# Kernel tuning notes

Hardware: AMD Instinct MI355X
Metric: run time of the kernel (lower is better)

## Reference

```python
import jax, jax.numpy as jnp
import numpy as np

B, N, INC, H, W = 1, 6, 256, 56, 100
DD, CC = 41, 64                         # depth bins (4..45 step 1), cam feat channels
NX, NY, NZ = 33, 33, 2                  # BEV grid from pc_range=[-50,-50,-5,50,50,3], grid=3
CZ = CC * NZ                            # 128 channels into bevencode
DXV = jnp.array([3.0, 3.0, 3.0], jnp.float32)
BXV = jnp.array([-48.5, -48.5, -3.5], jnp.float32)


def _frustum():
    ds = jnp.arange(4.0, 45.0, 1.0)                      # (41,)
    xs = jnp.linspace(0.0, 1599.0, W)
    ys = jnp.linspace(0.0, 899.0, H)
    d = jnp.broadcast_to(ds[:, None, None], (DD, H, W))
    xg = jnp.broadcast_to(xs[None, None, :], (DD, H, W))
    yg = jnp.broadcast_to(ys[None, :, None], (DD, H, W))
    return jnp.stack([xg, yg, d], -1)                    # (D,H,W,3)


def _conv(x, w):
    return jax.lax.conv_general_dilated(x, w, (1, 1), 'SAME',
                                        dimension_numbers=('NCHW', 'OIHW', 'NCHW'))


def _bn_relu(x, s, b, m, v):
    inv = s / jnp.sqrt(v + 1e-5)
    return jax.nn.relu(x * inv[None, :, None, None] + (b - m * inv)[None, :, None, None])


def _forward(x, rots, trans, dn_w, dn_b,
             bw1, bn1_s, bn1_b, bn1_m, bn1_v,
             bw2, bn2_s, bn2_b, bn2_m, bn2_v,
             bw3, bn3_s, bn3_b, bn3_m, bn3_v,
             bw4, bn4_s, bn4_b, bn4_m, bn4_v):
    # ---- CamEncode: 1x1 depthnet -> softmax depth dist + context features ----
    xf = x.reshape(B * N, INC, H, W)
    y = _conv(xf, dn_w) + dn_b[None, :, None, None]
    depth = jax.nn.softmax(y[:, :DD], axis=1).reshape(B, N, DD, H, W)
    feat = y[:, DD:DD + CC].reshape(B, N, CC, H, W)
    # ---- get_geometry: (u*d, v*d, d) -> ego frame ----
    fr = _frustum()                                                     # (D,H,W,3)
    pts = jnp.concatenate([fr[..., :2] * fr[..., 2:3], fr[..., 2:3]], -1)
    geom = jnp.einsum('bnij,dhwj->bndhwi', rots, pts) + trans[:, :, None, None, None, :]
    # ---- voxel indices (torch .long() truncates toward zero) ----
    coor = ((geom - (BXV - DXV / 2.0)) / DXV).astype(jnp.int32)         # (B,N,D,H,W,3)
    cx, cy, cz = coor[..., 0], coor[..., 1], coor[..., 2]
    kept = (cx >= 0) & (cx < NX) & (cy >= 0) & (cy < NY) & (cz >= 0) & (cz < NZ)
    bidx = jnp.arange(B, dtype=jnp.int32)[:, None, None, None, None]
    ranks = ((bidx * NZ + cz) * NY + cy) * NX + cx                      # bev rank per point
    nvox = B * NZ * NY * NX
    seg = jnp.where(kept, ranks, nvox).reshape(-1)                      # drop bucket = nvox
    # ---- lift: depth-weighted outer product, splat: segment-sum by voxel ----
    vol = depth[..., None] * feat.transpose(0, 1, 3, 4, 2)[:, :, None]  # (B,N,D,H,W,C)
    bev = jax.ops.segment_sum(vol.reshape(-1, CC), seg, num_segments=nvox + 1)[:nvox]
    bev = bev.reshape(B, NZ, NY, NX, CC).transpose(0, 4, 1, 2, 3).reshape(B, CZ, NY, NX)
    h = _bn_relu(_conv(bev, bw1), bn1_s, bn1_b, bn1_m, bn1_v)
    h = _bn_relu(_conv(h, bw2), bn2_s, bn2_b, bn2_m, bn2_v)
    h = _bn_relu(_conv(h, bw3), bn3_s, bn3_b, bn3_m, bn3_v)
    h = _bn_relu(_conv(h, bw4), bn4_s, bn4_b, bn4_m, bn4_v)
    return h                                                            # (B,256,33,33)


def setup_inputs() -> dict:
    key = jax.random.key(0)
    ks = jax.random.split(key, 16)
    x = jax.random.normal(ks[0], (B, N, INC, H, W), jnp.float32)
    # rots = small rotation perturbation composed with intrinsics inverse
    kinv = jnp.array([[1.0 / 800.0, 0.0, -1.0], [0.0, 1.0 / 800.0, -0.5625], [0.0, 0.0, 1.0]], jnp.float32)
    R = jnp.eye(3, dtype=jnp.float32) + 0.05 * jax.random.normal(ks[1], (B, N, 3, 3), jnp.float32)
    rots = jnp.einsum('bnij,jk->bnik', R, kinv)
    trans = 2.0 * jax.random.normal(ks[2], (B, N, 3), jnp.float32)

    def w(k, o, i, kh, kw):
        return jax.random.normal(k, (o, i, kh, kw), jnp.float32) * (2.0 / (i * kh * kw)) ** 0.5

    def bn(k, c):
        k1, k2, k3, k4 = jax.random.split(k, 4)
        return (1.0 + 0.1 * jax.random.normal(k1, (c,), jnp.float32),
                0.1 * jax.random.normal(k2, (c,), jnp.float32),
                0.1 * jax.random.normal(k3, (c,), jnp.float32),
                jax.random.uniform(k4, (c,), jnp.float32, 0.5, 1.5))
    bn1 = bn(ks[7], CZ); bn2 = bn(ks[8], 512); bn3 = bn(ks[9], 512); bn4 = bn(ks[10], 256)
    return dict(
        x=x, rots=rots, trans=trans,
        dn_w=w(ks[3], DD + CC, INC, 1, 1), dn_b=jnp.zeros((DD + CC,), jnp.float32),
        bw1=w(ks[4], CZ, CZ, 3, 3),
        bn1_s=bn1[0], bn1_b=bn1[1], bn1_m=bn1[2], bn1_v=bn1[3],
        bw2=w(ks[5], 512, CZ, 3, 3),
        bn2_s=bn2[0], bn2_b=bn2[1], bn2_m=bn2[2], bn2_v=bn2[3],
        bw3=w(ks[6], 512, 512, 3, 3),
        bn3_s=bn3[0], bn3_b=bn3[1], bn3_m=bn3[2], bn3_v=bn3[3],
        bw4=w(ks[11], 256, 512, 3, 3),
        bn4_s=bn4[0], bn4_b=bn4[1], bn4_m=bn4[2], bn4_v=bn4[3])


def reference(x, rots, trans, dn_w, dn_b,
              bw1, bn1_s, bn1_b, bn1_m, bn1_v,
              bw2, bn2_s, bn2_b, bn2_m, bn2_v,
              bw3, bn3_s, bn3_b, bn3_m, bn3_v,
              bw4, bn4_s, bn4_b, bn4_m, bn4_v):
    return _forward(x, rots, trans, dn_w, dn_b,
                    bw1, bn1_s, bn1_b, bn1_m, bn1_v,
                    bw2, bn2_s, bn2_b, bn2_m, bn2_v,
                    bw3, bn3_s, bn3_b, bn3_m, bn3_v,
                    bw4, bn4_s, bn4_b, bn4_m, bn4_v)
```

## Files before the change

kernel.cpp:

```cpp
#include <hip/hip_runtime.h>
#include <math.h>

#define NCAM  6
#define INC   256
#define HH    56
#define WW    100
#define HW    5600
#define NPIX  33600
#define DDEP  41
#define CFEAT 64
#define NCH   105
#define NXG   33
#define NYG   33
#define NZG   2
#define NVOX  2178
#define PADW  35
#define PADHW 1225
#define NPIXO 1089

typedef short bf16x8 __attribute__((ext_vector_type(8)));
typedef float f32x4  __attribute__((ext_vector_type(4)));

#define Y_OFF    0
#define YW_SZ    3538944
#define W3H_OFF  (Y_OFF)
#define W3L_OFF  (W3H_OFF + 1179648)
#define W4H_OFF  (W3L_OFF + 1179648)
#define W4L_OFF  (W4H_OFF + 589824)
#define W12_OFF  (Y_OFF + YW_SZ)
#define W1H_OFF  (W12_OFF)
#define W1L_OFF  (W1H_OFF + 73728)
#define W2H_OFF  (W1L_OFF + 73728)
#define W2L_OFF  (W2H_OFF + 294912)
#define BEV_OFF  (W2L_OFF + 294912)
#define BEV_SZ   (NVOX * CFEAT)
#define A0H_OFF  (BEV_OFF + BEV_SZ)
#define A0L_OFF  (A0H_OFF + 78400)
#define A1H_OFF  (A0L_OFF + 78400)
#define A1L_OFF  (A1H_OFF + 78400)
#define A2H_OFF  (A1L_OFF + 78400)
#define A2L_OFF  (A2H_OFF + 313600)
#define A3H_OFF  (A2L_OFF + 313600)
#define A3L_OFF  (A3H_OFF + 313600)
#define P_OFF    (A3L_OFF + 313600)
#define P_SZ     4460544
#define WS_END   (P_OFF + P_SZ)
#define WDH_OFF  (P_OFF)
#define WDL_OFF  (P_OFF + 16384)

__device__ __forceinline__ unsigned short f2bf_rn(float f) {
    unsigned u = __builtin_bit_cast(unsigned, f);
    unsigned r = (u + 0x7FFFu + ((u >> 16) & 1u)) >> 16;
    return (unsigned short)r;
}
__device__ __forceinline__ void split_bf(float f, unsigned short& h, unsigned short& l) {
    h = f2bf_rn(f);
    float hf = __builtin_bit_cast(float, (unsigned)h << 16);
    l = f2bf_rn(f - hf);
}

__global__ __launch_bounds__(256) void k_wprep_dn(const float* __restrict__ dnw,
                                                  unsigned short* __restrict__ wdh,
                                                  unsigned short* __restrict__ wdl)
{
    int i = blockIdx.x * 256 + threadIdx.x;
    if (i >= 128 * 256) return;
    int jj = i & 7, lane = (i >> 3) & 63, chk = (i >> 9) & 7, ct = i >> 12;
    int co = ct * 16 + (lane & 15);
    int ci = chk * 32 + (lane >> 4) * 8 + jj;
    float w = (co < NCH) ? dnw[co * 256 + ci] : 0.f;
    unsigned short h, l; split_bf(w, h, l);
    wdh[i] = h; wdl[i] = l;
}

__global__ __launch_bounds__(256) void k_depthnet_direct(const float* __restrict__ x,
                                                         const unsigned short* __restrict__ wdh,
                                                         const unsigned short* __restrict__ wdl,
                                                         const float* __restrict__ dnb,
                                                         float* __restrict__ y)
{
    const int t  = threadIdx.x;
    const int w  = t >> 6;
    const int l  = t & 63;
    const int lp = l & 15;
    const int q  = l >> 4;
    const int n   = blockIdx.y;
    const int ct0 = blockIdx.z * 4;
    const int px  = blockIdx.x * 64 + w * 16 + lp;
    const bool pok = px < HW;
    const float* xl = x + (size_t)n * INC * HW + (pok ? px : 0);

    f32x4 acc[4];
#pragma unroll
    for (int ct = 0; ct < 4; ++ct) acc[ct] = (f32x4){0.f, 0.f, 0.f, 0.f};

#pragma unroll 2
    for (int ci0 = 0; ci0 < INC; ci0 += 32) {
        float bv[8];
#pragma unroll
        for (int jj = 0; jj < 8; ++jj)
            bv[jj] = xl[(size_t)(ci0 + q * 8 + jj) * HW];
        bf16x8 Bh, Bl;
#pragma unroll
        for (int jj = 0; jj < 8; ++jj) {
            unsigned short h, lo; split_bf(pok ? bv[jj] : 0.f, h, lo);
            Bh[jj] = (short)h; Bl[jj] = (short)lo;
        }
#pragma unroll
        for (int ct = 0; ct < 4; ++ct) {
            const size_t ab = (size_t)(((ct0 + ct) * 8 + (ci0 >> 5)) * 64 + l) * 8;
            bf16x8 Ah = *(const bf16x8*)&wdh[ab];
            bf16x8 Al = *(const bf16x8*)&wdl[ab];
            acc[ct] = __builtin_amdgcn_mfma_f32_16x16x32_bf16(Ah, Bh, acc[ct], 0, 0, 0);
            acc[ct] = __builtin_amdgcn_mfma_f32_16x16x32_bf16(Ah, Bl, acc[ct], 0, 0, 0);
            acc[ct] = __builtin_amdgcn_mfma_f32_16x16x32_bf16(Al, Bh, acc[ct], 0, 0, 0);
        }
    }
    if (pok) {
#pragma unroll
        for (int ct = 0; ct < 4; ++ct) {
#pragma unroll
            for (int j = 0; j < 4; ++j) {
                int co = (ct0 + ct) * 16 + q * 4 + j;
                if (co < NCH)
                    y[((size_t)n * NCH + co) * HW + px] = acc[ct][j] + dnb[co];
            }
        }
    }
}

__global__ __launch_bounds__(256) void k_softmax(float* __restrict__ y)
{
    int p = blockIdx.x * 256 + threadIdx.x;
    if (p >= NPIX) return;
    int n = p / HW, hw = p - n * HW;
    float* base = y + (size_t)n * NCH * HW + hw;
    float v[DDEP];
    float m = -3.4e38f;
#pragma unroll
    for (int d = 0; d < DDEP; ++d) { v[d] = base[(size_t)d * HW]; m = fmaxf(m, v[d]); }
    float s = 0.f;
#pragma unroll
    for (int d = 0; d < DDEP; ++d) { v[d] = expf(v[d] - m); s += v[d]; }
#pragma unroll
    for (int d = 0; d < DDEP; ++d) base[(size_t)d * HW] = v[d] / s;
}

__global__ __launch_bounds__(256) void k_splat(const float* __restrict__ y,
                                               const float* __restrict__ rots,
                                               const float* __restrict__ trans,
                                               float* __restrict__ bev)
{
    int idx = blockIdx.x * 256 + threadIdx.x;
    if (idx >= NPIX * DDEP) return;
    int di = idx / NPIX;
    int p  = idx - di * NPIX;
    int n = p / HW, hw = p - n * HW;
    int wi = hw % WW, hi = hw / WW;
    const float su = 1599.0f / 99.0f;
    const float sv = 899.0f / 55.0f;
    float u = __fmul_rn((float)wi, su);
    float v = __fmul_rn((float)hi, sv);
    const float* r = rots + n * 9;
    const float* tr = trans + n * 3;
    float dd  = 4.0f + (float)di;
    float pxv = __fmul_rn(u, dd);
    float pyv = __fmul_rn(v, dd);
    float gx = __fadd_rn(__fadd_rn(__fadd_rn(__fmul_rn(r[0], pxv), __fmul_rn(r[1], pyv)), __fmul_rn(r[2], dd)), tr[0]);
    float gy = __fadd_rn(__fadd_rn(__fadd_rn(__fmul_rn(r[3], pxv), __fmul_rn(r[4], pyv)), __fmul_rn(r[5], dd)), tr[1]);
    float gz = __fadd_rn(__fadd_rn(__fadd_rn(__fmul_rn(r[6], pxv), __fmul_rn(r[7], pyv)), __fmul_rn(r[8], dd)), tr[2]);
    int cx = (int)__fdiv_rn(__fadd_rn(gx, 50.0f), 3.0f);
    int cy = (int)__fdiv_rn(__fadd_rn(gy, 50.0f), 3.0f);
    int cz = (int)__fdiv_rn(__fadd_rn(gz, 5.0f), 3.0f);
    if (cx >= 0 && cx < NXG && cy >= 0 && cy < NYG && cz >= 0 && cz < NZG) {
        const float* dbase = y + (size_t)n * NCH * HW + hw;
        const float* fbase = dbase + (size_t)DDEP * HW;
        float dval = dbase[(size_t)di * HW];
        float* vp = bev + (size_t)((cz * NYG + cy) * NXG + cx) * CFEAT;
#pragma unroll 8
        for (int c = 0; c < CFEAT; ++c) {
            atomicAdd(vp + c, __fmul_rn(dval, fbase[(size_t)c * HW]));
        }
    }
}

__global__ __launch_bounds__(256) void k_wprep(const float* __restrict__ wgt,
                                               unsigned short* __restrict__ wh,
                                               unsigned short* __restrict__ wl,
                                               int COUT, int CIN)
{
    int i = blockIdx.x * 256 + threadIdx.x;
    int total = 9 * COUT * CIN;
    if (i >= total) return;
    int jj = i & 7, lane = (i >> 3) & 63;
    int r  = i >> 9;
    int nchk = CIN >> 5;
    int chk = r % nchk; r /= nchk;
    int ncog = COUT >> 4;
    int cog = r % ncog; int dydx = r / ncog;
    int co = cog * 16 + (lane & 15);
    int ci = chk * 32 + (lane >> 4) * 8 + jj;
    float w = wgt[((size_t)co * CIN + ci) * 9 + dydx];
    unsigned short h, l; split_bf(w, h, l);
    wh[i] = h; wl[i] = l;
}

__global__ __launch_bounds__(256) void k_bev2act(const float* __restrict__ bev,
                                                 unsigned short* __restrict__ ah,
                                                 unsigned short* __restrict__ al)
{
    int i = blockIdx.x * 256 + threadIdx.x;
    if (i >= NVOX * CFEAT) return;
    int vx = i >> 6, c = i & 63;
    int cz = vx / NPIXO, rem = vx - cz * NPIXO;
    int yy = rem / NXG, xx = rem - yy * NXG;
    int ch = c * 2 + cz;
    int pos = (yy + 1) * PADW + xx + 1;
    unsigned short h, l; split_bf(bev[i], h, l);
    ah[pos * 128 + ch] = h;
    al[pos * 128 + ch] = l;
}

template<int CIN, int COUT, int SL>
__global__ __launch_bounds__(256) void k_conv_mfma(const unsigned short* __restrict__ ah,
                                                   const unsigned short* __restrict__ al,
                                                   const unsigned short* __restrict__ wh,
                                                   const unsigned short* __restrict__ wl,
                                                   float* __restrict__ P)
{
    constexpr int CI_PER = CIN / SL;
    constexpr int NCOB = COUT / 64;
    constexpr int G    = NCOB * SL;
    constexpr int GX   = G / 8;
    constexpr int POSN = 140;
    __shared__ unsigned short bs[POSN * 64];
    const int t  = threadIdx.x;
    const int w  = t >> 6;
    const int l  = t & 63;
    const int lp = l & 15;
    const int q  = l >> 4;

    const int bid   = blockIdx.x;
    const int xcd   = bid & 7;
    const int slot  = bid >> 3;
    const int ytile = slot % 17;
    const int gon   = slot / 17;
    const int group = xcd * GX + gon;
    const int cobi  = group % NCOB;
    const int sl    = group / NCOB;

    const int y0  = ytile * 2;
    const int cob = cobi * 64 + w * 16;
    const int ci_base = sl * CI_PER;

    int  pos0[5];
    bool vld[5];
#pragma unroll
    for (int ct = 0; ct < 5; ++ct) {
        int tp = ct * 16 + lp;
        int r = tp / 33, c = tp - r * 33;
        bool v = (tp < 66) && (y0 + r < 33);
        vld[ct]  = v;
        pos0[ct] = v ? (r * 35 + c) : 0;
    }

    f32x4 acc[5];
#pragma unroll
    for (int ct = 0; ct < 5; ++ct) acc[ct] = (f32x4){0.f, 0.f, 0.f, 0.f};

    for (int chk = 0; chk < CI_PER; chk += 32) {
        const int ci0 = ci_base + chk;
        __syncthreads();
        for (int i = t; i < POSN * 8; i += 256) {
            int pos = i >> 3, s = i & 7;
            int gpos = y0 * 35 + pos;
            const unsigned short* src = (s < 4) ? ah : al;
            int sp = s ^ (pos & 7);
            uint4 val = make_uint4(0u, 0u, 0u, 0u);
            if (gpos < PADHW)
                val = *(const uint4*)&src[(size_t)gpos * CIN + ci0 + (s & 3) * 8];
            *(uint4*)&bs[pos * 64 + sp * 8] = val;
        }
        __syncthreads();

#pragma unroll 3
        for (int dydx = 0; dydx < 9; ++dydx) {
            int dy = dydx / 3, dx = dydx - dy * 3;
            int off = dy * 35 + dx;
            const size_t abase = (size_t)(((dydx * (COUT >> 4) + (cob >> 4)) * (CIN >> 5)
                                           + (ci0 >> 5)) * 64 + l) * 8;
            bf16x8 Ah = *(const bf16x8*)&wh[abase];
            bf16x8 Al = *(const bf16x8*)&wl[abase];
#pragma unroll
            for (int ct = 0; ct < 5; ++ct) {
                int pos = pos0[ct] + off;
                int sph = q ^ (pos & 7);
                bf16x8 Bh = *(const bf16x8*)&bs[pos * 64 + sph * 8];
                bf16x8 Bl = *(const bf16x8*)&bs[pos * 64 + (sph ^ 4) * 8];
                acc[ct] = __builtin_amdgcn_mfma_f32_16x16x32_bf16(Ah, Bh, acc[ct], 0, 0, 0);
                acc[ct] = __builtin_amdgcn_mfma_f32_16x16x32_bf16(Ah, Bl, acc[ct], 0, 0, 0);
                acc[ct] = __builtin_amdgcn_mfma_f32_16x16x32_bf16(Al, Bh, acc[ct], 0, 0, 0);
            }
        }
    }

#pragma unroll
    for (int ct = 0; ct < 5; ++ct) {
        if (!vld[ct]) continue;
        int gp = y0 * 33 + ct * 16 + lp;
        float* dst = P + ((size_t)sl * NPIXO + gp) * COUT + cob + q * 4;
        *(f32x4*)dst = acc[ct];
    }
}

template<int SL>
__global__ __launch_bounds__(256) void k_finish(const float* __restrict__ P,
                                                const float* __restrict__ bns,
                                                const float* __restrict__ bnb,
                                                const float* __restrict__ bnm,
                                                const float* __restrict__ bnv,
                                                unsigned short* __restrict__ oh,
                                                unsigned short* __restrict__ ol,
                                                float* __restrict__ outf,
                                                int COUT)
{
    int i = blockIdx.x * 256 + threadIdx.x;
    if (i >= COUT * NPIXO) return;
    int co = i % COUT, p = i / COUT;
    float s = 0.f;
#pragma unroll
    for (int sl = 0; sl < SL; ++sl)
        s += P[((size_t)sl * NPIXO + p) * COUT + co];
    float sc = bns[co] / sqrtf(bnv[co] + 1e-5f);
    float bi = bnb[co] - bnm[co] * sc;
    float rv = fmaxf(fmaf(s, sc, bi), 0.f);
    if (outf) {
        outf[(size_t)co * NPIXO + p] = rv;
    } else {
        int yy = p / NXG, xx = p - yy * NXG;
        int pos = (yy + 1) * PADW + xx + 1;
        unsigned short h, lo; split_bf(rv, h, lo);
        oh[(size_t)pos * COUT + co] = h;
        ol[(size_t)pos * COUT + co] = lo;
    }
}

extern "C" void kernel_launch(void* const* d_in, const int* in_sizes, int n_in,
                              void* d_out, int out_size, void* d_ws, size_t ws_size,
                              hipStream_t stream)
{
    const float* x     = (const float*)d_in[0];
    const float* rots  = (const float*)d_in[1];
    const float* trans = (const float*)d_in[2];
    const float* dnw   = (const float*)d_in[3];
    const float* dnb   = (const float*)d_in[4];
    const float* bw1   = (const float*)d_in[5];
    const float* bn1s  = (const float*)d_in[6];
    const float* bn1b  = (const float*)d_in[7];
    const float* bn1m  = (const float*)d_in[8];
    const float* bn1v  = (const float*)d_in[9];
    const float* bw2   = (const float*)d_in[10];
    const float* bn2s  = (const float*)d_in[11];
    const float* bn2b  = (const float*)d_in[12];
    const float* bn2m  = (const float*)d_in[13];
    const float* bn2v  = (const float*)d_in[14];
    const float* bw3   = (const float*)d_in[15];
    const float* bn3s  = (const float*)d_in[16];
    const float* bn3b  = (const float*)d_in[17];
    const float* bn3m  = (const float*)d_in[18];
    const float* bn3v  = (const float*)d_in[19];
    const float* bw4   = (const float*)d_in[20];
    const float* bn4s  = (const float*)d_in[21];
    const float* bn4b  = (const float*)d_in[22];
    const float* bn4m  = (const float*)d_in[23];
    const float* bn4v  = (const float*)d_in[24];

    float* ws  = (float*)d_ws;
    float* y   = ws + Y_OFF;
    float* bev = ws + BEV_OFF;
    float* P   = ws + P_OFF;
    unsigned short* w1h = (unsigned short*)(ws + W1H_OFF);
    unsigned short* w1l = (unsigned short*)(ws + W1L_OFF);
    unsigned short* w2h = (unsigned short*)(ws + W2H_OFF);
    unsigned short* w2l = (unsigned short*)(ws + W2L_OFF);
    unsigned short* w3h = (unsigned short*)(ws + W3H_OFF);
    unsigned short* w3l = (unsigned short*)(ws + W3L_OFF);
    unsigned short* w4h = (unsigned short*)(ws + W4H_OFF);
    unsigned short* w4l = (unsigned short*)(ws + W4L_OFF);
    unsigned short* a0h = (unsigned short*)(ws + A0H_OFF);
    unsigned short* a0l = (unsigned short*)(ws + A0L_OFF);
    unsigned short* a1h = (unsigned short*)(ws + A1H_OFF);
    unsigned short* a1l = (unsigned short*)(ws + A1L_OFF);
    unsigned short* a2h = (unsigned short*)(ws + A2H_OFF);
    unsigned short* a2l = (unsigned short*)(ws + A2L_OFF);
    unsigned short* a3h = (unsigned short*)(ws + A3H_OFF);
    unsigned short* a3l = (unsigned short*)(ws + A3L_OFF);
    unsigned short* wdh = (unsigned short*)(ws + WDH_OFF);
    unsigned short* wdl = (unsigned short*)(ws + WDL_OFF);
    float* out = (float*)d_out;

    hipMemsetAsync(bev, 0, (size_t)(P_OFF - BEV_OFF) * sizeof(float), stream);

    k_wprep_dn<<<128, 256, 0, stream>>>(dnw, wdh, wdl);
    k_depthnet_direct<<<dim3(88, 6, 2), 256, 0, stream>>>(x, wdh, wdl, dnb, y);
    k_softmax<<<132, 256, 0, stream>>>(y);
    k_splat<<<(NPIX * DDEP + 255) / 256, 256, 0, stream>>>(y, rots, trans, bev);

    k_wprep<<<(9 * 128 * 128 + 255) / 256, 256, 0, stream>>>(bw1, w1h, w1l, 128, 128);
    k_wprep<<<(9 * 512 * 128 + 255) / 256, 256, 0, stream>>>(bw2, w2h, w2l, 512, 128);
    k_wprep<<<(9 * 512 * 512 + 255) / 256, 256, 0, stream>>>(bw3, w3h, w3l, 512, 512);
    k_wprep<<<(9 * 256 * 512 + 255) / 256, 256, 0, stream>>>(bw4, w4h, w4l, 256, 512);

    k_bev2act<<<(NVOX * CFEAT + 255) / 256, 256, 0, stream>>>(bev, a0h, a0l);

    k_conv_mfma<128, 128, 4><<<136, 256, 0, stream>>>(a0h, a0l, w1h, w1l, P);
    k_finish<4><<<(128 * NPIXO + 255) / 256, 256, 0, stream>>>(P, bn1s, bn1b, bn1m, bn1v, a1h, a1l, nullptr, 128);
    k_conv_mfma<128, 512, 4><<<544, 256, 0, stream>>>(a1h, a1l, w2h, w2l, P);
    k_finish<4><<<(512 * NPIXO + 255) / 256, 256, 0, stream>>>(P, bn2s, bn2b, bn2m, bn2v, a2h, a2l, nullptr, 512);
    k_conv_mfma<512, 512, 8><<<1088, 256, 0, stream>>>(a2h, a2l, w3h, w3l, P);
    k_finish<8><<<(512 * NPIXO + 255) / 256, 256, 0, stream>>>(P, bn3s, bn3b, bn3m, bn3v, a3h, a3l, nullptr, 512);
    k_conv_mfma<512, 256, 8><<<544, 256, 0, stream>>>(a3h, a3l, w4h, w4l, P);
    k_finish<8><<<(256 * NPIXO + 255) / 256, 256, 0, stream>>>(P, bn4s, bn4b, bn4m, bn4v, nullptr, nullptr, out, 256);
}
```

Before: 144.7 us.

## Fuse softmax into depthnet, batch weight prep, and run-merge splat atomics

New measurement: 134.9 us. 1.07x faster.

```diff
diff --git a/kernel.cpp b/kernel.cpp
--- a/kernel.cpp
+++ b/kernel.cpp
@@ -22,17 +22,18 @@
 typedef float f32x4  __attribute__((ext_vector_type(4)));
 
 #define Y_OFF    0
-#define YW_SZ    3538944
-#define W3H_OFF  (Y_OFF)
+#define Y_SZ     (NCAM * NCH * HW)
+#define WDH_OFF  (Y_OFF + Y_SZ)
+#define WDL_OFF  (WDH_OFF + 16384)
+#define W1H_OFF  (WDL_OFF + 16384)
+#define W1L_OFF  (W1H_OFF + 73728)
+#define W2H_OFF  (W1L_OFF + 73728)
+#define W2L_OFF  (W2H_OFF + 294912)
+#define W3H_OFF  (W2L_OFF + 294912)
 #define W3L_OFF  (W3H_OFF + 1179648)
 #define W4H_OFF  (W3L_OFF + 1179648)
 #define W4L_OFF  (W4H_OFF + 589824)
-#define W12_OFF  (Y_OFF + YW_SZ)
-#define W1H_OFF  (W12_OFF)
-#define W1L_OFF  (W1H_OFF + 73728)
-#define W2H_OFF  (W1L_OFF + 73728)
-#define W2L_OFF  (W2H_OFF + 294912)
-#define BEV_OFF  (W2L_OFF + 294912)
+#define BEV_OFF  (W4L_OFF + 589824)
 #define BEV_SZ   (NVOX * CFEAT)
 #define A0H_OFF  (BEV_OFF + BEV_SZ)
 #define A0L_OFF  (A0H_OFF + 78400)
@@ -45,8 +46,6 @@
 #define P_OFF    (A3L_OFF + 313600)
 #define P_SZ     4460544
 #define WS_END   (P_OFF + P_SZ)
-#define WDH_OFF  (P_OFF)
-#define WDL_OFF  (P_OFF + 16384)
 
 __device__ __forceinline__ unsigned short f2bf_rn(float f) {
     unsigned u = __builtin_bit_cast(unsigned, f);
@@ -59,139 +58,11 @@
     l = f2bf_rn(f - hf);
 }
 
-__global__ __launch_bounds__(256) void k_wprep_dn(const float* __restrict__ dnw,
-                                                  unsigned short* __restrict__ wdh,
-                                                  unsigned short* __restrict__ wdl)
-{
-    int i = blockIdx.x * 256 + threadIdx.x;
-    if (i >= 128 * 256) return;
-    int jj = i & 7, lane = (i >> 3) & 63, chk = (i >> 9) & 7, ct = i >> 12;
-    int co = ct * 16 + (lane & 15);
-    int ci = chk * 32 + (lane >> 4) * 8 + jj;
-    float w = (co < NCH) ? dnw[co * 256 + ci] : 0.f;
-    unsigned short h, l; split_bf(w, h, l);
-    wdh[i] = h; wdl[i] = l;
-}
-
-__global__ __launch_bounds__(256) void k_depthnet_direct(const float* __restrict__ x,
-                                                         const unsigned short* __restrict__ wdh,
-                                                         const unsigned short* __restrict__ wdl,
-                                                         const float* __restrict__ dnb,
-                                                         float* __restrict__ y)
-{
-    const int t  = threadIdx.x;
-    const int w  = t >> 6;
-    const int l  = t & 63;
-    const int lp = l & 15;
-    const int q  = l >> 4;
-    const int n   = blockIdx.y;
-    const int ct0 = blockIdx.z * 4;
-    const int px  = blockIdx.x * 64 + w * 16 + lp;
-    const bool pok = px < HW;
-    const float* xl = x + (size_t)n * INC * HW + (pok ? px : 0);
-
-    f32x4 acc[4];
-#pragma unroll
-    for (int ct = 0; ct < 4; ++ct) acc[ct] = (f32x4){0.f, 0.f, 0.f, 0.f};
-
-#pragma unroll 2
-    for (int ci0 = 0; ci0 < INC; ci0 += 32) {
-        float bv[8];
-#pragma unroll
-        for (int jj = 0; jj < 8; ++jj)
-            bv[jj] = xl[(size_t)(ci0 + q * 8 + jj) * HW];
-        bf16x8 Bh, Bl;
-#pragma unroll
-        for (int jj = 0; jj < 8; ++jj) {
-            unsigned short h, lo; split_bf(pok ? bv[jj] : 0.f, h, lo);
-            Bh[jj] = (short)h; Bl[jj] = (short)lo;
-        }
-#pragma unroll
-        for (int ct = 0; ct < 4; ++ct) {
-            const size_t ab = (size_t)(((ct0 + ct) * 8 + (ci0 >> 5)) * 64 + l) * 8;
-            bf16x8 Ah = *(const bf16x8*)&wdh[ab];
-            bf16x8 Al = *(const bf16x8*)&wdl[ab];
-            acc[ct] = __builtin_amdgcn_mfma_f32_16x16x32_bf16(Ah, Bh, acc[ct], 0, 0, 0);
-            acc[ct] = __builtin_amdgcn_mfma_f32_16x16x32_bf16(Ah, Bl, acc[ct], 0, 0, 0);
-            acc[ct] = __builtin_amdgcn_mfma_f32_16x16x32_bf16(Al, Bh, acc[ct], 0, 0, 0);
-        }
-    }
-    if (pok) {
-#pragma unroll
-        for (int ct = 0; ct < 4; ++ct) {
-#pragma unroll
-            for (int j = 0; j < 4; ++j) {
-                int co = (ct0 + ct) * 16 + q * 4 + j;
-                if (co < NCH)
-                    y[((size_t)n * NCH + co) * HW + px] = acc[ct][j] + dnb[co];
-            }
-        }
-    }
-}
-
-__global__ __launch_bounds__(256) void k_softmax(float* __restrict__ y)
-{
-    int p = blockIdx.x * 256 + threadIdx.x;
-    if (p >= NPIX) return;
-    int n = p / HW, hw = p - n * HW;
-    float* base = y + (size_t)n * NCH * HW + hw;
-    float v[DDEP];
-    float m = -3.4e38f;
-#pragma unroll
-    for (int d = 0; d < DDEP; ++d) { v[d] = base[(size_t)d * HW]; m = fmaxf(m, v[d]); }
-    float s = 0.f;
-#pragma unroll
-    for (int d = 0; d < DDEP; ++d) { v[d] = expf(v[d] - m); s += v[d]; }
-#pragma unroll
-    for (int d = 0; d < DDEP; ++d) base[(size_t)d * HW] = v[d] / s;
-}
-
-__global__ __launch_bounds__(256) void k_splat(const float* __restrict__ y,
-                                               const float* __restrict__ rots,
-                                               const float* __restrict__ trans,
-                                               float* __restrict__ bev)
-{
-    int idx = blockIdx.x * 256 + threadIdx.x;
-    if (idx >= NPIX * DDEP) return;
-    int di = idx / NPIX;
-    int p  = idx - di * NPIX;
-    int n = p / HW, hw = p - n * HW;
-    int wi = hw % WW, hi = hw / WW;
-    const float su = 1599.0f / 99.0f;
-    const float sv = 899.0f / 55.0f;
-    float u = __fmul_rn((float)wi, su);
-    float v = __fmul_rn((float)hi, sv);
-    const float* r = rots + n * 9;
-    const float* tr = trans + n * 3;
-    float dd  = 4.0f + (float)di;
-    float pxv = __fmul_rn(u, dd);
-    float pyv = __fmul_rn(v, dd);
-    float gx = __fadd_rn(__fadd_rn(__fadd_rn(__fmul_rn(r[0], pxv), __fmul_rn(r[1], pyv)), __fmul_rn(r[2], dd)), tr[0]);
-    float gy = __fadd_rn(__fadd_rn(__fadd_rn(__fmul_rn(r[3], pxv), __fmul_rn(r[4], pyv)), __fmul_rn(r[5], dd)), tr[1]);
-    float gz = __fadd_rn(__fadd_rn(__fadd_rn(__fmul_rn(r[6], pxv), __fmul_rn(r[7], pyv)), __fmul_rn(r[8], dd)), tr[2]);
-    int cx = (int)__fdiv_rn(__fadd_rn(gx, 50.0f), 3.0f);
-    int cy = (int)__fdiv_rn(__fadd_rn(gy, 50.0f), 3.0f);
-    int cz = (int)__fdiv_rn(__fadd_rn(gz, 5.0f), 3.0f);
-    if (cx >= 0 && cx < NXG && cy >= 0 && cy < NYG && cz >= 0 && cz < NZG) {
-        const float* dbase = y + (size_t)n * NCH * HW + hw;
-        const float* fbase = dbase + (size_t)DDEP * HW;
-        float dval = dbase[(size_t)di * HW];
-        float* vp = bev + (size_t)((cz * NYG + cy) * NXG + cx) * CFEAT;
-#pragma unroll 8
-        for (int c = 0; c < CFEAT; ++c) {
-            atomicAdd(vp + c, __fmul_rn(dval, fbase[(size_t)c * HW]));
-        }
-    }
-}
-
-__global__ __launch_bounds__(256) void k_wprep(const float* __restrict__ wgt,
-                                               unsigned short* __restrict__ wh,
-                                               unsigned short* __restrict__ wl,
-                                               int COUT, int CIN)
-{
-    int i = blockIdx.x * 256 + threadIdx.x;
-    int total = 9 * COUT * CIN;
-    if (i >= total) return;
+__device__ __forceinline__ void wprep_conv(const float* __restrict__ wgt,
+                                           unsigned short* __restrict__ wh,
+                                           unsigned short* __restrict__ wl,
+                                           int COUT, int CIN, int i)
+{
     int jj = i & 7, lane = (i >> 3) & 63;
     int r  = i >> 9;
     int nchk = CIN >> 5;
@@ -203,6 +74,216 @@
     float w = wgt[((size_t)co * CIN + ci) * 9 + dydx];
     unsigned short h, l; split_bf(w, h, l);
     wh[i] = h; wl[i] = l;
+}
+
+__global__ __launch_bounds__(256) void k_wprep_all(const float* __restrict__ dnw,
+                                                   const float* __restrict__ bw1,
+                                                   const float* __restrict__ bw2,
+                                                   const float* __restrict__ bw3,
+                                                   const float* __restrict__ bw4,
+                                                   unsigned short* __restrict__ wdh,
+                                                   unsigned short* __restrict__ wdl,
+                                                   unsigned short* __restrict__ w1h,
+                                                   unsigned short* __restrict__ w1l,
+                                                   unsigned short* __restrict__ w2h,
+                                                   unsigned short* __restrict__ w2l,
+                                                   unsigned short* __restrict__ w3h,
+                                                   unsigned short* __restrict__ w3l,
+                                                   unsigned short* __restrict__ w4h,
+                                                   unsigned short* __restrict__ w4l)
+{
+    int i = blockIdx.x * 256 + threadIdx.x;
+    if (i < 32768) {
+        int jj = i & 7, lane = (i >> 3) & 63, chk = (i >> 9) & 7, ct = i >> 12;
+        int co = ct * 16 + (lane & 15);
+        int ci = chk * 32 + (lane >> 4) * 8 + jj;
+        float w = (co < NCH) ? dnw[co * 256 + ci] : 0.f;
+        unsigned short h, l; split_bf(w, h, l);
+        wdh[i] = h; wdl[i] = l;
+        return;
+    }
+    i -= 32768;
+    if (i < 147456)  { wprep_conv(bw1, w1h, w1l, 128, 128, i); return; }
+    i -= 147456;
+    if (i < 589824)  { wprep_conv(bw2, w2h, w2l, 512, 128, i); return; }
+    i -= 589824;
+    if (i < 2359296) { wprep_conv(bw3, w3h, w3l, 512, 512, i); return; }
+    i -= 2359296;
+    if (i < 1179648) { wprep_conv(bw4, w4h, w4l, 256, 512, i); return; }
+}
+
+__global__ __launch_bounds__(256) void k_depthnet_fused(const float* __restrict__ x,
+                                                        const unsigned short* __restrict__ wdh,
+                                                        const unsigned short* __restrict__ wdl,
+                                                        const float* __restrict__ dnb,
+                                                        float* __restrict__ y)
+{
+    const int t  = threadIdx.x;
+    const int w  = t >> 6;
+    const int l  = t & 63;
+    const int lp = l & 15;
+    const int q  = l >> 4;
+    const int n   = blockIdx.y;
+    const int ct0 = blockIdx.z * 4;
+    const int px  = blockIdx.x * 64 + w * 16 + lp;
+    const bool pok = px < HW;
+    const float* xl = x + (size_t)n * INC * HW + (pok ? px : 0);
+
+    f32x4 acc[4];
+#pragma unroll
+    for (int ct = 0; ct < 4; ++ct) acc[ct] = (f32x4){0.f, 0.f, 0.f, 0.f};
+
+#pragma unroll 2
+    for (int ci0 = 0; ci0 < INC; ci0 += 32) {
+        float bv[8];
+#pragma unroll
+        for (int jj = 0; jj < 8; ++jj)
+            bv[jj] = xl[(size_t)(ci0 + q * 8 + jj) * HW];
+        bf16x8 Bh, Bl;
+#pragma unroll
+        for (int jj = 0; jj < 8; ++jj) {
+            unsigned short h, lo; split_bf(pok ? bv[jj] : 0.f, h, lo);
+            Bh[jj] = (short)h; Bl[jj] = (short)lo;
+        }
+#pragma unroll
+        for (int ct = 0; ct < 4; ++ct) {
+            const size_t ab = (size_t)(((ct0 + ct) * 8 + (ci0 >> 5)) * 64 + l) * 8;
+            bf16x8 Ah = *(const bf16x8*)&wdh[ab];
+            bf16x8 Al = *(const bf16x8*)&wdl[ab];
+            acc[ct] = __builtin_amdgcn_mfma_f32_16x16x32_bf16(Ah, Bh, acc[ct], 0, 0, 0);
+            acc[ct] = __builtin_amdgcn_mfma_f32_16x16x32_bf16(Ah, Bl, acc[ct], 0, 0, 0);
+            acc[ct] = __builtin_amdgcn_mfma_f32_16x16x32_bf16(Al, Bh, acc[ct], 0, 0, 0);
+        }
+    }
+
+    float v[4][4];
+#pragma unroll
+    for (int ct = 0; ct < 4; ++ct)
+#pragma unroll
+        for (int j = 0; j < 4; ++j) {
+            int co = (ct0 + ct) * 16 + q * 4 + j;
+            v[ct][j] = acc[ct][j] + ((co < NCH) ? dnb[co] : 0.f);
+        }
+
+    if (ct0 == 0) {
+        float m = -3.4e38f;
+#pragma unroll
+        for (int ct = 0; ct < 4; ++ct)
+#pragma unroll
+            for (int j = 0; j < 4; ++j) {
+                int co = ct * 16 + q * 4 + j;
+                if (co < DDEP) m = fmaxf(m, v[ct][j]);
+            }
+        m = fmaxf(m, __shfl_xor(m, 16));
+        m = fmaxf(m, __shfl_xor(m, 32));
+        float e[4][4];
+        float s = 0.f;
+#pragma unroll
+        for (int ct = 0; ct < 4; ++ct)
+#pragma unroll
+            for (int j = 0; j < 4; ++j) {
+                int co = ct * 16 + q * 4 + j;
+                e[ct][j] = (co < DDEP) ? expf(v[ct][j] - m) : 0.f;
+                s += e[ct][j];
+            }
+        s += __shfl_xor(s, 16);
+        s += __shfl_xor(s, 32);
+#pragma unroll
+        for (int ct = 0; ct < 4; ++ct)
+#pragma unroll
+            for (int j = 0; j < 4; ++j) {
+                int co = ct * 16 + q * 4 + j;
+                if (co < DDEP) v[ct][j] = e[ct][j] / s;
+            }
+    }
+
+    if (pok) {
+#pragma unroll
+        for (int ct = 0; ct < 4; ++ct)
+#pragma unroll
+            for (int j = 0; j < 4; ++j) {
+                int co = (ct0 + ct) * 16 + q * 4 + j;
+                if (co < NCH)
+                    y[((size_t)n * NCH + co) * HW + px] = v[ct][j];
+            }
+    }
+}
+
+__global__ __launch_bounds__(256) void k_splat2(const float* __restrict__ y,
+                                                const float* __restrict__ rots,
+                                                const float* __restrict__ trans,
+                                                float* __restrict__ bev)
+{
+    __shared__ int vox[32 * DDEP];
+    const int t  = threadIdx.x;
+    const int p0 = blockIdx.x * 32;
+
+    for (int k = t; k < 32 * DDEP; k += 256) {
+        int pl = k / DDEP, d = k - pl * DDEP;
+        int p = p0 + pl;
+        int vx = -1;
+        {
+            int n = p / HW, hw = p - n * HW;
+            int wi = hw % WW, hi = hw / WW;
+            const float su = 1599.0f / 99.0f;
+            const float sv = 899.0f / 55.0f;
+            float u = __fmul_rn((float)wi, su);
+            float v = __fmul_rn((float)hi, sv);
+            const float* r = rots + n * 9;
+            const float* tr = trans + n * 3;
+            float dd  = 4.0f + (float)d;
+            float pxv = __fmul_rn(u, dd);
+            float pyv = __fmul_rn(v, dd);
+            float gx = __fadd_rn(__fadd_rn(__fadd_rn(__fmul_rn(r[0], pxv), __fmul_rn(r[1], pyv)), __fmul_rn(r[2], dd)), tr[0]);
+            float gy = __fadd_rn(__fadd_rn(__fadd_rn(__fmul_rn(r[3], pxv), __fmul_rn(r[4], pyv)), __fmul_rn(r[5], dd)), tr[1]);
+            float gz = __fadd_rn(__fadd_rn(__fadd_rn(__fmul_rn(r[6], pxv), __fmul_rn(r[7], pyv)), __fmul_rn(r[8], dd)), tr[2]);
+            int cx = (int)__fdiv_rn(__fadd_rn(gx, 50.0f), 3.0f);
+            int cy = (int)__fdiv_rn(__fadd_rn(gy, 50.0f), 3.0f);
+            int cz = (int)__fdiv_rn(__fadd_rn(gz, 5.0f), 3.0f);
+            if (cx >= 0 && cx < NXG && cy >= 0 && cy < NYG && cz >= 0 && cz < NZG)
+                vx = (cz * NYG + cy) * NXG + cx;
+        }
+        vox[k] = vx;
+    }
+    __syncthreads();
+
+    const int g  = t >> 5;
+    const int pl = t & 31;
+    const int p  = p0 + pl;
+    int n = p / HW, hw = p - n * HW;
+    const float* dbase = y + (size_t)n * NCH * HW + hw;
+    const float* fbase = dbase + (size_t)DDEP * HW;
+    float f[8];
+#pragma unroll
+    for (int j = 0; j < 8; ++j) f[j] = fbase[(size_t)(g * 8 + j) * HW];
+
+    float a[8];
+#pragma unroll
+    for (int j = 0; j < 8; ++j) a[j] = 0.f;
+    int cur = -1;
+    for (int d = 0; d < DDEP; ++d) {
+        int vx = vox[pl * DDEP + d];
+        if (vx != cur) {
+            if (cur >= 0) {
+                float* vp = bev + (size_t)cur * CFEAT + g * 8;
+#pragma unroll
+                for (int j = 0; j < 8; ++j) atomicAdd(vp + j, a[j]);
+            }
+            cur = vx;
+#pragma unroll
+            for (int j = 0; j < 8; ++j) a[j] = 0.f;
+        }
+        if (vx >= 0) {
+            float dval = dbase[(size_t)d * HW];
+#pragma unroll
+            for (int j = 0; j < 8; ++j) a[j] += __fmul_rn(dval, f[j]);
+        }
+    }
+    if (cur >= 0) {
+        float* vp = bev + (size_t)cur * CFEAT + g * 8;
+#pragma unroll
+        for (int j = 0; j < 8; ++j) atomicAdd(vp + j, a[j]);
+    }
 }
 
 __global__ __launch_bounds__(256) void k_bev2act(const float* __restrict__ bev,
@@ -379,6 +460,8 @@
     float* y   = ws + Y_OFF;
     float* bev = ws + BEV_OFF;
     float* P   = ws + P_OFF;
+    unsigned short* wdh = (unsigned short*)(ws + WDH_OFF);
+    unsigned short* wdl = (unsigned short*)(ws + WDL_OFF);
     unsigned short* w1h = (unsigned short*)(ws + W1H_OFF);
     unsigned short* w1l = (unsigned short*)(ws + W1L_OFF);
     unsigned short* w2h = (unsigned short*)(ws + W2H_OFF);
@@ -395,21 +478,15 @@
     unsigned short* a2l = (unsigned short*)(ws + A2L_OFF);
     unsigned short* a3h = (unsigned short*)(ws + A3H_OFF);
     unsigned short* a3l = (unsigned short*)(ws + A3L_OFF);
-    unsigned short* wdh = (unsigned short*)(ws + WDH_OFF);
-    unsigned short* wdl = (unsigned short*)(ws + WDL_OFF);
     float* out = (float*)d_out;
 
     hipMemsetAsync(bev, 0, (size_t)(P_OFF - BEV_OFF) * sizeof(float), stream);
 
-    k_wprep_dn<<<128, 256, 0, stream>>>(dnw, wdh, wdl);
-    k_depthnet_direct<<<dim3(88, 6, 2), 256, 0, stream>>>(x, wdh, wdl, dnb, y);
-    k_softmax<<<132, 256, 0, stream>>>(y);
-    k_splat<<<(NPIX * DDEP + 255) / 256, 256, 0, stream>>>(y, rots, trans, bev);
-
-    k_wprep<<<(9 * 128 * 128 + 255) / 256, 256, 0, stream>>>(bw1, w1h, w1l, 128, 128);
-    k_wprep<<<(9 * 512 * 128 + 255) / 256, 256, 0, stream>>>(bw2, w2h, w2l, 512, 128);
-    k_wprep<<<(9 * 512 * 512 + 255) / 256, 256, 0, stream>>>(bw3, w3h, w3l, 512, 512);
-    k_wprep<<<(9 * 256 * 512 + 255) / 256, 256, 0, stream>>>(bw4, w4h, w4l, 256, 512);
+    k_wprep_all<<<16832, 256, 0, stream>>>(dnw, bw1, bw2, bw3, bw4,
+                                           wdh, wdl, w1h, w1l, w2h, w2l,
+                                           w3h, w3l, w4h, w4l);
+    k_depthnet_fused<<<dim3(88, 6, 2), 256, 0, stream>>>(x, wdh, wdl, dnb, y);
+    k_splat2<<<1050, 256, 0, stream>>>(y, rots, trans, bev);
 
     k_bev2act<<<(NVOX * CFEAT + 255) / 256, 256, 0, stream>>>(bev, a0h, a0l);
 
```
